# Kernel tuning notes

Measured on AMD Instinct MI355X. Metric: run time of the kernel, lower is better.

Reference implementation:

```python
import jax, jax.numpy as jnp
import numpy as np

N_EMBD = 1024
N_HEAD = 16
HEAD_DIM = N_EMBD // N_HEAD
B, T = 4, 2048


def setup_inputs() -> dict:
    key = jax.random.key(0)
    ks = jax.random.split(key, 5)
    s_in = 1.0 / np.sqrt(N_EMBD)
    return {
        "x": jax.random.normal(ks[0], (B, T, N_EMBD), dtype=jnp.float32),
        "w_attn": jax.random.normal(ks[1], (N_EMBD, 3 * N_EMBD), dtype=jnp.float32) * s_in,
        "b_attn": jnp.zeros((3 * N_EMBD,), dtype=jnp.float32),
        "w_proj": jax.random.normal(ks[2], (N_EMBD, N_EMBD), dtype=jnp.float32) * s_in,
        "b_proj": jnp.zeros((N_EMBD,), dtype=jnp.float32),
    }


def reference(x, w_attn, b_attn, w_proj, b_proj):
    b, t, c = x.shape
    qkv = x @ w_attn + b_attn                      # [B,T,3C]
    q, k, v = jnp.split(qkv, 3, axis=-1)
    # [B,T,C] -> [B,H,T,D]
    def heads(z):
        return z.reshape(b, t, N_HEAD, HEAD_DIM).transpose(0, 2, 1, 3)
    q, k, v = heads(q), heads(k), heads(v)
    scale = 1.0 / np.sqrt(HEAD_DIM)
    att = jnp.einsum("bhqd,bhkd->bhqk", q, k) * scale
    causal = jnp.tril(jnp.ones((t, t), dtype=bool))
    att = jnp.where(causal, att, -jnp.inf)
    att = jax.nn.softmax(att, axis=-1)
    y = jnp.einsum("bhqk,bhkd->bhqd", att, v)      # [B,H,T,D]
    y = y.transpose(0, 2, 1, 3).reshape(b, t, c)
    return y @ w_proj + b_proj
```

## Files before the change

### kernel.cpp

```cpp
#include <hip/hip_runtime.h>
#include <hip/hip_bf16.h>

#define B_  4
#define T_  2048
#define C_  1024
#define H_  16
#define D_  64
#define C3_ 3072

typedef __attribute__((ext_vector_type(8))) short bf16x8;
typedef __attribute__((ext_vector_type(4))) float f32x4;
typedef unsigned short u16;

#define CSCALE 0.1803368801111204f

__device__ __forceinline__ u16 f2bf(float f) {
  union { float f; unsigned int u; } v; v.f = f;
  unsigned int r = (v.u + 0x7FFFu + ((v.u >> 16) & 1u)) >> 16;
  return (u16)r;
}

__device__ __forceinline__ void gload16(void* l, const void* g) {
  __builtin_amdgcn_global_load_lds(
      (const __attribute__((address_space(1))) unsigned int*)g,
      (__attribute__((address_space(3))) unsigned int*)l, 16, 0, 0);
}

__global__ __launch_bounds__(256)
void cvt_bf16(const float* __restrict__ in, u16* __restrict__ out, int n8) {
  int i = blockIdx.x * 256 + threadIdx.x;
  if (i >= n8) return;
  float4 a = *(const float4*)(in + (size_t)i * 8);
  float4 b = *(const float4*)(in + (size_t)i * 8 + 4);
  ushort4 lo, hi;
  lo.x = f2bf(a.x); lo.y = f2bf(a.y); lo.z = f2bf(a.z); lo.w = f2bf(a.w);
  hi.x = f2bf(b.x); hi.y = f2bf(b.y); hi.z = f2bf(b.z); hi.w = f2bf(b.w);
  *(ushort4*)(out + (size_t)i * 8) = lo;
  *(ushort4*)(out + (size_t)i * 8 + 4) = hi;
}

__global__ __launch_bounds__(256)
void transcvt(const float* __restrict__ w, u16* __restrict__ wT, int K, int N) {
  int n  = blockIdx.x * 64 + (threadIdx.x & 63);
  int k0 = blockIdx.y * 16 + (threadIdx.x >> 6) * 4;
  float v0 = w[(size_t)(k0 + 0) * N + n];
  float v1 = w[(size_t)(k0 + 1) * N + n];
  float v2 = w[(size_t)(k0 + 2) * N + n];
  float v3 = w[(size_t)(k0 + 3) * N + n];
  ushort4 o; o.x = f2bf(v0); o.y = f2bf(v1); o.z = f2bf(v2); o.w = f2bf(v3);
  *(ushort4*)(wT + (size_t)n * K + k0) = o;
}

__global__ __launch_bounds__(256)
void vtrans(const u16* __restrict__ qkv, u16* __restrict__ vT) {
  const int bid = blockIdx.x;
  const int bh = bid >> 6, tc = bid & 63;
  const int d = threadIdx.x & 63, t4 = threadIdx.x >> 6;
  const int t8 = tc * 4 + t4;
  const int b = bh >> 4, h = bh & 15;
  const u16* src = qkv + (size_t)(b * T_ + t8 * 8) * C3_ + 2 * C_ + h * 64 + d;
  union { u16 a[8]; int4 v; } u;
#pragma unroll
  for (int e = 0; e < 8; ++e) u.a[e] = src[(size_t)e * C3_];
  *(int4*)(vT + ((size_t)bh * 64 + d) * T_ + t8 * 8) = u.v;
}

template <typename OutT, int BM>
__global__ __launch_bounds__(512, 2)
void gemm256(const u16* __restrict__ A, const u16* __restrict__ Bt,
             const float* __restrict__ bias, OutT* __restrict__ C,
             int M, int N, int K, int qscale_cols) {
  constexpr int AG = BM * 8;
  constexpr int S  = AG + 2048;
  constexpr int MF = BM / 64;
  constexpr int ALOADS = BM / 128;
  __shared__ int4 lds[2 * S];

  const int tid = threadIdx.x, lane = tid & 63, wid = tid >> 6;
  const int wr = wid >> 2, wc = wid & 3;
  const int row0 = blockIdx.y * BM, col0 = blockIdx.x * 256;

  f32x4 acc[2 * MF][4];
#pragma unroll
  for (int m = 0; m < 2 * MF; ++m)
#pragma unroll
    for (int nf = 0; nf < 4; ++nf) acc[m][nf] = (f32x4){0.f, 0.f, 0.f, 0.f};

  const u16* pA[2][ALOADS]; const u16* pB[2][2];
#pragma unroll
  for (int h = 0; h < 2; ++h) {
#pragma unroll
    for (int i = 0; i < ALOADS; ++i) {
      int g = h * (AG / 2) + i * 512 + tid;
      int rr = ((g >> 7) << 4) + (g & 15), ko = ((g >> 4) & 7) * 8;
      pA[h][i] = A + (size_t)(row0 + rr) * K + ko;
    }
#pragma unroll
    for (int i = 0; i < 2; ++i) {
      int g = h * 1024 + i * 512 + tid;
      int rr = ((g >> 7) << 4) + (g & 15), ko = ((g >> 4) & 7) * 8;
      pB[h][i] = Bt + (size_t)(col0 + rr) * K + ko;
    }
  }

  auto stage = [&](int t, int isA, int h, int buf) {
    if (isA) {
      int4* d = &lds[buf * S + h * (AG / 2) + wid * 64];
      gload16(d, pA[h][0] + t * 64);
      if constexpr (ALOADS == 2) gload16(d + 512, pA[h][1] + t * 64);
    } else {
      int4* d = &lds[buf * S + AG + h * 1024 + wid * 64];
      gload16(d, pB[h][0] + t * 64);
      gload16(d + 512, pB[h][1] + t * 64);
    }
  };
  auto rdA = [&](int f, int kk, int buf) {
    return *(const bf16x8*)&lds[buf * S + (wr * (2 * MF) + f) * 128 + kk * 64 + lane];
  };
  auto rdB = [&](int nf, int kk, int buf) {
    return *(const bf16x8*)&lds[buf * S + AG + (wc * 4 + nf) * 128 + kk * 64 + lane];
  };

#define WAIT_KEEP() do { if constexpr (BM == 256) \
    asm volatile("s_waitcnt vmcnt(6)" ::: "memory"); else \
    asm volatile("s_waitcnt vmcnt(5)" ::: "memory"); } while (0)

  const int nk = K >> 6, nit = nk >> 1;

  stage(0, 1, 0, 0); stage(0, 1, 1, 0); stage(0, 0, 0, 0); stage(0, 0, 1, 0);
  stage(1, 0, 0, 1); stage(1, 0, 1, 1); stage(1, 1, 0, 1);
  WAIT_KEEP();
  __builtin_amdgcn_s_barrier();

  for (int it = 0; it < nit; ++it) {
    const int t1g = 2 * it + 1, t2g = t1g + 1, t3g = t1g + 2;
    bf16x8 a0[MF][2], a1[MF][2], b0[2][2], b1[2][2];

#pragma unroll
    for (int m = 0; m < MF; ++m) { a0[m][0] = rdA(m, 0, 0); a0[m][1] = rdA(m, 1, 0); }
#pragma unroll
    for (int nf = 0; nf < 2; ++nf) { b0[nf][0] = rdB(nf, 0, 0); b0[nf][1] = rdB(nf, 1, 0); }
    stage(t1g, 1, 1, 1);
    __builtin_amdgcn_s_barrier();
    __builtin_amdgcn_s_setprio(1);
#pragma unroll
    for (int m = 0; m < MF; ++m)
#pragma unroll
      for (int nf = 0; nf < 2; ++nf) {
        acc[m][nf] = __builtin_amdgcn_mfma_f32_16x16x32_bf16(a0[m][0], b0[nf][0], acc[m][nf], 0, 0, 0);
        acc[m][nf] = __builtin_amdgcn_mfma_f32_16x16x32_bf16(a0[m][1], b0[nf][1], acc[m][nf], 0, 0, 0);
      }
    __builtin_amdgcn_s_setprio(0);
    __builtin_amdgcn_s_barrier();

#pragma unroll
    for (int nf = 0; nf < 2; ++nf) { b1[nf][0] = rdB(2 + nf, 0, 0); b1[nf][1] = rdB(2 + nf, 1, 0); }
    __builtin_amdgcn_s_barrier();
    __builtin_amdgcn_s_setprio(1);
#pragma unroll
    for (int m = 0; m < MF; ++m)
#pragma unroll
      for (int nf = 0; nf < 2; ++nf) {
        acc[m][2 + nf] = __builtin_amdgcn_mfma_f32_16x16x32_bf16(a0[m][0], b1[nf][0], acc[m][2 + nf], 0, 0, 0);
        acc[m][2 + nf] = __builtin_amdgcn_mfma_f32_16x16x32_bf16(a0[m][1], b1[nf][1], acc[m][2 + nf], 0, 0, 0);
      }
    __builtin_amdgcn_s_setprio(0);
    __builtin_amdgcn_s_barrier();

#pragma unroll
    for (int m = 0; m < MF; ++m) { a1[m][0] = rdA(MF + m, 0, 0); a1[m][1] = rdA(MF + m, 1, 0); }
    if (t2g < nk) stage(t2g, 0, 0, 0);
    __builtin_amdgcn_s_barrier();
    __builtin_amdgcn_s_setprio(1);
#pragma unroll
    for (int m = 0; m < MF; ++m)
#pragma unroll
      for (int nf = 0; nf < 2; ++nf) {
        acc[MF + m][2 + nf] = __builtin_amdgcn_mfma_f32_16x16x32_bf16(a1[m][0], b1[nf][0], acc[MF + m][2 + nf], 0, 0, 0);
        acc[MF + m][2 + nf] = __builtin_amdgcn_mfma_f32_16x16x32_bf16(a1[m][1], b1[nf][1], acc[MF + m][2 + nf], 0, 0, 0);
      }
    __builtin_amdgcn_s_setprio(0);
    __builtin_amdgcn_s_barrier();

    if (t2g < nk) {
      stage(t2g, 0, 1, 0);
      stage(t2g, 1, 0, 0);
      WAIT_KEEP();
    } else {
      asm volatile("s_waitcnt vmcnt(0)" ::: "memory");
    }
    __builtin_amdgcn_s_barrier();
    __builtin_amdgcn_s_setprio(1);
#pragma unroll
    for (int m = 0; m < MF; ++m)
#pragma unroll
      for (int nf = 0; nf < 2; ++nf) {
        acc[MF + m][nf] = __builtin_amdgcn_mfma_f32_16x16x32_bf16(a1[m][0], b0[nf][0], acc[MF + m][nf], 0, 0, 0);
        acc[MF + m][nf] = __builtin_amdgcn_mfma_f32_16x16x32_bf16(a1[m][1], b0[nf][1], acc[MF + m][nf], 0, 0, 0);
      }
    __builtin_amdgcn_s_setprio(0);
    __builtin_amdgcn_s_barrier();

#pragma unroll
    for (int m = 0; m < MF; ++m) { a0[m][0] = rdA(m, 0, 1); a0[m][1] = rdA(m, 1, 1); }
#pragma unroll
    for (int nf = 0; nf < 2; ++nf) { b0[nf][0] = rdB(nf, 0, 1); b0[nf][1] = rdB(nf, 1, 1); }
    if (t2g < nk) stage(t2g, 1, 1, 0);
    __builtin_amdgcn_s_barrier();
    __builtin_amdgcn_s_setprio(1);
#pragma unroll
    for (int m = 0; m < MF; ++m)
#pragma unroll
      for (int nf = 0; nf < 2; ++nf) {
        acc[m][nf] = __builtin_amdgcn_mfma_f32_16x16x32_bf16(a0[m][0], b0[nf][0], acc[m][nf], 0, 0, 0);
        acc[m][nf] = __builtin_amdgcn_mfma_f32_16x16x32_bf16(a0[m][1], b0[nf][1], acc[m][nf], 0, 0, 0);
      }
    __builtin_amdgcn_s_setprio(0);
    __builtin_amdgcn_s_barrier();

#pragma unroll
    for (int nf = 0; nf < 2; ++nf) { b1[nf][0] = rdB(2 + nf, 0, 1); b1[nf][1] = rdB(2 + nf, 1, 1); }
    __builtin_amdgcn_s_barrier();
    __builtin_amdgcn_s_setprio(1);
#pragma unroll
    for (int m = 0; m < MF; ++m)
#pragma unroll
      for (int nf = 0; nf < 2; ++nf) {
        acc[m][2 + nf] = __builtin_amdgcn_mfma_f32_16x16x32_bf16(a0[m][0], b1[nf][0], acc[m][2 + nf], 0, 0, 0);
        acc[m][2 + nf] = __builtin_amdgcn_mfma_f32_16x16x32_bf16(a0[m][1], b1[nf][1], acc[m][2 + nf], 0, 0, 0);
      }
    __builtin_amdgcn_s_setprio(0);
    __builtin_amdgcn_s_barrier();

#pragma unroll
    for (int m = 0; m < MF; ++m) { a1[m][0] = rdA(MF + m, 0, 1); a1[m][1] = rdA(MF + m, 1, 1); }
    if (t3g < nk) stage(t3g, 0, 0, 1);
    __builtin_amdgcn_s_barrier();
    __builtin_amdgcn_s_setprio(1);
#pragma unroll
    for (int m = 0; m < MF; ++m)
#pragma unroll
      for (int nf = 0; nf < 2; ++nf) {
        acc[MF + m][2 + nf] = __builtin_amdgcn_mfma_f32_16x16x32_bf16(a1[m][0], b1[nf][0], acc[MF + m][2 + nf], 0, 0, 0);
        acc[MF + m][2 + nf] = __builtin_amdgcn_mfma_f32_16x16x32_bf16(a1[m][1], b1[nf][1], acc[MF + m][2 + nf], 0, 0, 0);
      }
    __builtin_amdgcn_s_setprio(0);
    __builtin_amdgcn_s_barrier();

    if (t3g < nk) {
      stage(t3g, 0, 1, 1);
      stage(t3g, 1, 0, 1);
      WAIT_KEEP();
    } else {
      asm volatile("s_waitcnt vmcnt(0)" ::: "memory");
    }
    __builtin_amdgcn_s_barrier();
    __builtin_amdgcn_s_setprio(1);
#pragma unroll
    for (int m = 0; m < MF; ++m)
#pragma unroll
      for (int nf = 0; nf < 2; ++nf) {
        acc[MF + m][nf] = __builtin_amdgcn_mfma_f32_16x16x32_bf16(a1[m][0], b0[nf][0], acc[MF + m][nf], 0, 0, 0);
        acc[MF + m][nf] = __builtin_amdgcn_mfma_f32_16x16x32_bf16(a1[m][1], b0[nf][1], acc[MF + m][nf], 0, 0, 0);
      }
    __builtin_amdgcn_s_setprio(0);
    __builtin_amdgcn_s_barrier();
  }
#undef WAIT_KEEP

  const int cc = lane & 15, qg = lane >> 4;
#pragma unroll
  for (int m = 0; m < 2 * MF; ++m) {
#pragma unroll
    for (int nf = 0; nf < 4; ++nf) {
      const int gc = col0 + wc * 64 + nf * 16 + cc;
      const float bv = bias[gc];
      const float sc = (gc < qscale_cols) ? CSCALE : 1.0f;
#pragma unroll
      for (int r = 0; r < 4; ++r) {
        const int gr = row0 + wr * (BM / 2) + m * 16 + qg * 4 + r;
        float val = (acc[m][nf][r] + bv) * sc;
        if constexpr (sizeof(OutT) == 2)
          ((u16*)C)[(size_t)gr * N + gc] = f2bf(val);
        else
          ((float*)C)[(size_t)gr * N + gc] = val;
      }
    }
  }
}

__global__ __launch_bounds__(512, 4)
void attn_mfma(const u16* __restrict__ qkv, const u16* __restrict__ vT,
               u16* __restrict__ yout) {
  __shared__ int4 Ks4[512];
  __shared__ int4 Vs4[512];
  __shared__ int4 Ps4[2048];

  const int n   = blockIdx.x;
  const int xcd = n & 7, t = n >> 3;
  const int bh  = xcd * 8 + (t >> 3);
  const int ip  = t & 7;
  const int b   = bh >> 4, h = bh & 15;

  const int tid = threadIdx.x;
  const int lane = tid & 63, wq = tid >> 6;
  const int sub = wq & 3;
  const int cc = lane & 15, qg = lane >> 4;

  const int qt128 = (wq < 4) ? ip : (15 - ip);
  const int qrow0 = qt128 * 128 + sub * 32;
  const int diag  = qt128 * 2 + (sub >> 1);
  const int jn    = 32 - 2 * ip;

  const u16* kbase = qkv + (size_t)b * T_ * C3_ + C_ + h * D_;
  const u16* vtb   = vT + (size_t)bh * D_ * T_;

  bf16x8 qf[2][2];
#pragma unroll
  for (int hf = 0; hf < 2; ++hf) {
    const u16* qb = qkv + (size_t)(b * T_ + qrow0 + hf * 16 + cc) * C3_ + h * D_;
    qf[hf][0] = *(const bf16x8*)(qb + qg * 8);
    qf[hf][1] = *(const bf16x8*)(qb + 32 + qg * 8);
  }

  const u16* kg = kbase + (size_t)((tid >> 7) * 16 + (tid & 15)) * C3_ +
                  ((tid >> 6) & 1) * 32 + ((tid >> 4) & 3) * 8;
  const u16* vg = vtb + (size_t)((tid >> 7) * 16 + (tid & 15)) * T_ +
                  ((tid >> 6) & 1) * 32 + ((tid >> 4) & 3) * 8;

  int4 kpref = *(const int4*)kg;
  int4 vpref = *(const int4*)vg;

  float m_r[2] = {-1e30f, -1e30f}, l_r[2] = {0.f, 0.f};
  f32x4 o[2][4];
#pragma unroll
  for (int hf = 0; hf < 2; ++hf)
#pragma unroll
    for (int db = 0; db < 4; ++db) o[hf][db] = (f32x4){0.f, 0.f, 0.f, 0.f};

  for (int j = 0; j < jn; ++j) {
    __syncthreads();
    Ks4[tid] = kpref;
    Vs4[tid] = vpref;
    __syncthreads();
    if (j + 1 < jn) {
      kpref = *(const int4*)(kg + (size_t)(j + 1) * 64 * C3_);
      vpref = *(const int4*)(vg + (j + 1) * 64);
    }
    if (j > diag) continue;

    __builtin_amdgcn_s_setprio(1);
    f32x4 s[2][4];
#pragma unroll
    for (int kb = 0; kb < 4; ++kb) {
      bf16x8 kf0 = *(const bf16x8*)(Ks4 + kb * 128 + lane);
      bf16x8 kf1 = *(const bf16x8*)(Ks4 + kb * 128 + 64 + lane);
#pragma unroll
      for (int hf = 0; hf < 2; ++hf) {
        f32x4 z = (f32x4){0.f, 0.f, 0.f, 0.f};
        z = __builtin_amdgcn_mfma_f32_16x16x32_bf16(kf0, qf[hf][0], z, 0, 0, 0);
        z = __builtin_amdgcn_mfma_f32_16x16x32_bf16(kf1, qf[hf][1], z, 0, 0, 0);
        s[hf][kb] = z;
      }
    }
    __builtin_amdgcn_s_setprio(0);

    if (j == diag) {
#pragma unroll
      for (int hf = 0; hf < 2; ++hf) {
        const int qabs = qrow0 + hf * 16 + cc;
#pragma unroll
        for (int kb = 0; kb < 4; ++kb)
#pragma unroll
          for (int r = 0; r < 4; ++r)
            if ((j * 64 + kb * 16 + qg * 4 + r) > qabs) s[hf][kb][r] = -1e30f;
      }
    }

#pragma unroll
    for (int hf = 0; hf < 2; ++hf) {
      float mx = s[hf][0][0];
#pragma unroll
      for (int kb = 0; kb < 4; ++kb)
#pragma unroll
        for (int r = 0; r < 4; ++r) mx = fmaxf(mx, s[hf][kb][r]);
      mx = fmaxf(mx, __shfl_xor(mx, 16));
      mx = fmaxf(mx, __shfl_xor(mx, 32));

      if (!__all(mx <= m_r[hf])) {
        float mn = fmaxf(m_r[hf], mx);
        float al = exp2f(m_r[hf] - mn);
        m_r[hf] = mn;
        l_r[hf] *= al;
        float alq[4];
#pragma unroll
        for (int r = 0; r < 4; ++r)
          alq[r] = __shfl(al, (lane & 48) | (qg * 4 + r));
#pragma unroll
        for (int db = 0; db < 4; ++db)
#pragma unroll
          for (int r = 0; r < 4; ++r) o[hf][db][r] *= alq[r];
      }

      float lsum = 0.f;
#pragma unroll
      for (int kb = 0; kb < 4; ++kb)
#pragma unroll
        for (int r = 0; r < 4; ++r) {
          float p = exp2f(s[hf][kb][r] - m_r[hf]);
          s[hf][kb][r] = p;
          lsum += p;
        }
      l_r[hf] += lsum;

      char* myPb = (char*)(Ps4 + wq * 256 + hf * 128);
#pragma unroll
      for (int kb = 0; kb < 4; ++kb) {
        unsigned plo, phi;
        asm("v_cvt_pk_bf16_f32 %0, %1, %2" : "=v"(plo) : "v"(s[hf][kb][0]), "v"(s[hf][kb][1]));
        asm("v_cvt_pk_bf16_f32 %0, %1, %2" : "=v"(phi) : "v"(s[hf][kb][2]), "v"(s[hf][kb][3]));
        const int kv0 = kb * 16 + qg * 4;
        const int g = ((kv0 >> 5) << 6) + (((kv0 >> 3) & 3) << 4) + cc;
        uint2 pk; pk.x = plo; pk.y = phi;
        *(uint2*)(myPb + g * 16 + (kv0 & 7) * 2) = pk;
      }
    }

    bf16x8 pa[2][2];
#pragma unroll
    for (int hf = 0; hf < 2; ++hf)
#pragma unroll
      for (int ks = 0; ks < 2; ++ks)
        pa[hf][ks] = *(const bf16x8*)(Ps4 + wq * 256 + hf * 128 + ks * 64 + lane);
    __builtin_amdgcn_s_setprio(1);
#pragma unroll
    for (int db = 0; db < 4; ++db) {
#pragma unroll
      for (int ks = 0; ks < 2; ++ks) {
        bf16x8 vf = *(const bf16x8*)(Vs4 + db * 128 + ks * 64 + lane);
        o[0][db] = __builtin_amdgcn_mfma_f32_16x16x32_bf16(pa[0][ks], vf, o[0][db], 0, 0, 0);
        o[1][db] = __builtin_amdgcn_mfma_f32_16x16x32_bf16(pa[1][ks], vf, o[1][db], 0, 0, 0);
      }
    }
    __builtin_amdgcn_s_setprio(0);
  }

#pragma unroll
  for (int hf = 0; hf < 2; ++hf) {
    float ls = l_r[hf];
    ls += __shfl_xor(ls, 16);
    ls += __shfl_xor(ls, 32);
    float linv_l = 1.0f / ls;
    float linv[4];
#pragma unroll
    for (int r = 0; r < 4; ++r)
      linv[r] = __shfl(linv_l, (lane & 48) | (qg * 4 + r));

    u16* yb = yout + (size_t)(b * T_ + qrow0 + hf * 16 + qg * 4) * C_ + h * D_ + cc;
#pragma unroll
    for (int db = 0; db < 4; ++db)
#pragma unroll
      for (int r = 0; r < 4; ++r)
        yb[(size_t)r * C_ + db * 16] = f2bf(o[hf][db][r] * linv[r]);
  }
}

extern "C" void kernel_launch(void* const* d_in, const int* in_sizes, int n_in,
                              void* d_out, int out_size, void* d_ws, size_t ws_size,
                              hipStream_t stream) {
  const float* x      = (const float*)d_in[0];
  const float* w_attn = (const float*)d_in[1];
  const float* b_attn = (const float*)d_in[2];
  const float* w_proj = (const float*)d_in[3];
  const float* b_proj = (const float*)d_in[4];
  float* out = (float*)d_out;

  char* ws = (char*)d_ws;
  u16* xb  = (u16*)(ws);
  u16* waT = (u16*)(ws + 16777216);
  u16* wpT = (u16*)(ws + 23068672);
  u16* qkv = (u16*)(ws + 25165824);
  u16* yb  = (u16*)(ws + 75497472);
  u16* vT  = (u16*)(ws + 92274688);

  cvt_bf16<<<4096, 256, 0, stream>>>(x, xb, (B_ * T_ * C_) / 8);
  transcvt<<<dim3(C3_ / 64, C_ / 16), 256, 0, stream>>>(w_attn, waT, C_, C3_);
  transcvt<<<dim3(C_ / 64, C_ / 16), 256, 0, stream>>>(w_proj, wpT, C_, C_);

  gemm256<u16, 256><<<dim3(C3_ / 256, (B_ * T_) / 256), 512, 0, stream>>>(
      xb, waT, b_attn, qkv, B_ * T_, C3_, C_, C_);

  vtrans<<<4096, 256, 0, stream>>>(qkv, vT);

  attn_mfma<<<dim3(8 * H_ * B_), 512, 0, stream>>>(qkv, vT, yb);

  gemm256<float, 128><<<dim3(C_ / 256, (B_ * T_) / 128), 512, 0, stream>>>(
      yb, wpT, b_proj, out, B_ * T_, C_, C_, 0);
}
```

Before: 218.3 us.

## Double-buffer K/V tiles in LDS with direct global-to-LDS async loads

```diff
diff --git a/kernel.cpp b/kernel.cpp
--- a/kernel.cpp
+++ b/kernel.cpp
@@ -292,8 +292,8 @@
 __global__ __launch_bounds__(512, 4)
 void attn_mfma(const u16* __restrict__ qkv, const u16* __restrict__ vT,
                u16* __restrict__ yout) {
-  __shared__ int4 Ks4[512];
-  __shared__ int4 Vs4[512];
+  __shared__ int4 Ks4[2][512];
+  __shared__ int4 Vs4[2][512];
   __shared__ int4 Ps4[2048];
 
   const int n   = blockIdx.x;
@@ -328,9 +328,6 @@
   const u16* vg = vtb + (size_t)((tid >> 7) * 16 + (tid & 15)) * T_ +
                   ((tid >> 6) & 1) * 32 + ((tid >> 4) & 3) * 8;
 
-  int4 kpref = *(const int4*)kg;
-  int4 vpref = *(const int4*)vg;
-
   float m_r[2] = {-1e30f, -1e30f}, l_r[2] = {0.f, 0.f};
   f32x4 o[2][4];
 #pragma unroll
@@ -338,111 +335,116 @@
 #pragma unroll
     for (int db = 0; db < 4; ++db) o[hf][db] = (f32x4){0.f, 0.f, 0.f, 0.f};
 
+  gload16(&Ks4[0][wq * 64], kg);
+  gload16(&Vs4[0][wq * 64], vg);
+  __syncthreads();
+
   for (int j = 0; j < jn; ++j) {
+    const int p = j & 1;
+
+    if (j + 1 < jn) {
+      gload16(&Ks4[p ^ 1][wq * 64], kg + (size_t)(j + 1) * 64 * C3_);
+      gload16(&Vs4[p ^ 1][wq * 64], vg + (j + 1) * 64);
+    }
+
+    if (j <= diag) {
+      __builtin_amdgcn_s_setprio(1);
+      f32x4 s[2][4];
+#pragma unroll
+      for (int kb = 0; kb < 4; ++kb) {
+        bf16x8 kf0 = *(const bf16x8*)(&Ks4[p][0] + kb * 128 + lane);
+        bf16x8 kf1 = *(const bf16x8*)(&Ks4[p][0] + kb * 128 + 64 + lane);
+#pragma unroll
+        for (int hf = 0; hf < 2; ++hf) {
+          f32x4 z = (f32x4){0.f, 0.f, 0.f, 0.f};
+          z = __builtin_amdgcn_mfma_f32_16x16x32_bf16(kf0, qf[hf][0], z, 0, 0, 0);
+          z = __builtin_amdgcn_mfma_f32_16x16x32_bf16(kf1, qf[hf][1], z, 0, 0, 0);
+          s[hf][kb] = z;
+        }
+      }
+      __builtin_amdgcn_s_setprio(0);
+
+      if (j == diag) {
+#pragma unroll
+        for (int hf = 0; hf < 2; ++hf) {
+          const int qabs = qrow0 + hf * 16 + cc;
+#pragma unroll
+          for (int kb = 0; kb < 4; ++kb)
+#pragma unroll
+            for (int r = 0; r < 4; ++r)
+              if ((j * 64 + kb * 16 + qg * 4 + r) > qabs) s[hf][kb][r] = -1e30f;
+        }
+      }
+
+#pragma unroll
+      for (int hf = 0; hf < 2; ++hf) {
+        float m0 = fmaxf(fmaxf(s[hf][0][0], s[hf][0][1]), fmaxf(s[hf][0][2], s[hf][0][3]));
+        float m1 = fmaxf(fmaxf(s[hf][1][0], s[hf][1][1]), fmaxf(s[hf][1][2], s[hf][1][3]));
+        float m2 = fmaxf(fmaxf(s[hf][2][0], s[hf][2][1]), fmaxf(s[hf][2][2], s[hf][2][3]));
+        float m3 = fmaxf(fmaxf(s[hf][3][0], s[hf][3][1]), fmaxf(s[hf][3][2], s[hf][3][3]));
+        float mx = fmaxf(fmaxf(m0, m1), fmaxf(m2, m3));
+        mx = fmaxf(mx, __shfl_xor(mx, 16));
+        mx = fmaxf(mx, __shfl_xor(mx, 32));
+
+        if (!__all(mx <= m_r[hf])) {
+          float mn = fmaxf(m_r[hf], mx);
+          float al = exp2f(m_r[hf] - mn);
+          m_r[hf] = mn;
+          l_r[hf] *= al;
+          float alq[4];
+#pragma unroll
+          for (int r = 0; r < 4; ++r)
+            alq[r] = __shfl(al, (lane & 48) | (qg * 4 + r));
+#pragma unroll
+          for (int db = 0; db < 4; ++db)
+#pragma unroll
+            for (int r = 0; r < 4; ++r) o[hf][db][r] *= alq[r];
+        }
+
+#pragma unroll
+        for (int kb = 0; kb < 4; ++kb)
+#pragma unroll
+          for (int r = 0; r < 4; ++r)
+            s[hf][kb][r] = exp2f(s[hf][kb][r] - m_r[hf]);
+        float l0 = (s[hf][0][0] + s[hf][0][1]) + (s[hf][0][2] + s[hf][0][3]);
+        float l1 = (s[hf][1][0] + s[hf][1][1]) + (s[hf][1][2] + s[hf][1][3]);
+        float l2 = (s[hf][2][0] + s[hf][2][1]) + (s[hf][2][2] + s[hf][2][3]);
+        float l3 = (s[hf][3][0] + s[hf][3][1]) + (s[hf][3][2] + s[hf][3][3]);
+        l_r[hf] += (l0 + l1) + (l2 + l3);
+
+        char* myPb = (char*)(Ps4 + wq * 256 + hf * 128);
+#pragma unroll
+        for (int kb = 0; kb < 4; ++kb) {
+          unsigned plo, phi;
+          asm("v_cvt_pk_bf16_f32 %0, %1, %2" : "=v"(plo) : "v"(s[hf][kb][0]), "v"(s[hf][kb][1]));
+          asm("v_cvt_pk_bf16_f32 %0, %1, %2" : "=v"(phi) : "v"(s[hf][kb][2]), "v"(s[hf][kb][3]));
+          const int kv0 = kb * 16 + qg * 4;
+          const int g = ((kv0 >> 5) << 6) + (((kv0 >> 3) & 3) << 4) + cc;
+          uint2 pk; pk.x = plo; pk.y = phi;
+          *(uint2*)(myPb + g * 16 + (kv0 & 7) * 2) = pk;
+        }
+      }
+
+      bf16x8 pa[2][2];
+#pragma unroll
+      for (int hf = 0; hf < 2; ++hf)
+#pragma unroll
+        for (int ks = 0; ks < 2; ++ks)
+          pa[hf][ks] = *(const bf16x8*)(Ps4 + wq * 256 + hf * 128 + ks * 64 + lane);
+      __builtin_amdgcn_s_setprio(1);
+#pragma unroll
+      for (int db = 0; db < 4; ++db) {
+#pragma unroll
+        for (int ks = 0; ks < 2; ++ks) {
+          bf16x8 vf = *(const bf16x8*)(&Vs4[p][0] + db * 128 + ks * 64 + lane);
+          o[0][db] = __builtin_amdgcn_mfma_f32_16x16x32_bf16(pa[0][ks], vf, o[0][db], 0, 0, 0);
+          o[1][db] = __builtin_amdgcn_mfma_f32_16x16x32_bf16(pa[1][ks], vf, o[1][db], 0, 0, 0);
+        }
+      }
+      __builtin_amdgcn_s_setprio(0);
+    }
+
     __syncthreads();
-    Ks4[tid] = kpref;
-    Vs4[tid] = vpref;
-    __syncthreads();
-    if (j + 1 < jn) {
-      kpref = *(const int4*)(kg + (size_t)(j + 1) * 64 * C3_);
-      vpref = *(const int4*)(vg + (j + 1) * 64);
-    }
-    if (j > diag) continue;
-
-    __builtin_amdgcn_s_setprio(1);
-    f32x4 s[2][4];
-#pragma unroll
-    for (int kb = 0; kb < 4; ++kb) {
-      bf16x8 kf0 = *(const bf16x8*)(Ks4 + kb * 128 + lane);
-      bf16x8 kf1 = *(const bf16x8*)(Ks4 + kb * 128 + 64 + lane);
-#pragma unroll
-      for (int hf = 0; hf < 2; ++hf) {
-        f32x4 z = (f32x4){0.f, 0.f, 0.f, 0.f};
-        z = __builtin_amdgcn_mfma_f32_16x16x32_bf16(kf0, qf[hf][0], z, 0, 0, 0);
-        z = __builtin_amdgcn_mfma_f32_16x16x32_bf16(kf1, qf[hf][1], z, 0, 0, 0);
-        s[hf][kb] = z;
-      }
-    }
-    __builtin_amdgcn_s_setprio(0);
-
-    if (j == diag) {
-#pragma unroll
-      for (int hf = 0; hf < 2; ++hf) {
-        const int qabs = qrow0 + hf * 16 + cc;
-#pragma unroll
-        for (int kb = 0; kb < 4; ++kb)
-#pragma unroll
-          for (int r = 0; r < 4; ++r)
-            if ((j * 64 + kb * 16 + qg * 4 + r) > qabs) s[hf][kb][r] = -1e30f;
-      }
-    }
-
-#pragma unroll
-    for (int hf = 0; hf < 2; ++hf) {
-      float mx = s[hf][0][0];
-#pragma unroll
-      for (int kb = 0; kb < 4; ++kb)
-#pragma unroll
-        for (int r = 0; r < 4; ++r) mx = fmaxf(mx, s[hf][kb][r]);
-      mx = fmaxf(mx, __shfl_xor(mx, 16));
-      mx = fmaxf(mx, __shfl_xor(mx, 32));
-
-      if (!__all(mx <= m_r[hf])) {
-        float mn = fmaxf(m_r[hf], mx);
-        float al = exp2f(m_r[hf] - mn);
-        m_r[hf] = mn;
-        l_r[hf] *= al;
-        float alq[4];
-#pragma unroll
-        for (int r = 0; r < 4; ++r)
-          alq[r] = __shfl(al, (lane & 48) | (qg * 4 + r));
-#pragma unroll
-        for (int db = 0; db < 4; ++db)
-#pragma unroll
-          for (int r = 0; r < 4; ++r) o[hf][db][r] *= alq[r];
-      }
-
-      float lsum = 0.f;
-#pragma unroll
-      for (int kb = 0; kb < 4; ++kb)
-#pragma unroll
-        for (int r = 0; r < 4; ++r) {
-          float p = exp2f(s[hf][kb][r] - m_r[hf]);
-          s[hf][kb][r] = p;
-          lsum += p;
-        }
-      l_r[hf] += lsum;
-
-      char* myPb = (char*)(Ps4 + wq * 256 + hf * 128);
-#pragma unroll
-      for (int kb = 0; kb < 4; ++kb) {
-        unsigned plo, phi;
-        asm("v_cvt_pk_bf16_f32 %0, %1, %2" : "=v"(plo) : "v"(s[hf][kb][0]), "v"(s[hf][kb][1]));
-        asm("v_cvt_pk_bf16_f32 %0, %1, %2" : "=v"(phi) : "v"(s[hf][kb][2]), "v"(s[hf][kb][3]));
-        const int kv0 = kb * 16 + qg * 4;
-        const int g = ((kv0 >> 5) << 6) + (((kv0 >> 3) & 3) << 4) + cc;
-        uint2 pk; pk.x = plo; pk.y = phi;
-        *(uint2*)(myPb + g * 16 + (kv0 & 7) * 2) = pk;
-      }
-    }
-
-    bf16x8 pa[2][2];
-#pragma unroll
-    for (int hf = 0; hf < 2; ++hf)
-#pragma unroll
-      for (int ks = 0; ks < 2; ++ks)
-        pa[hf][ks] = *(const bf16x8*)(Ps4 + wq * 256 + hf * 128 + ks * 64 + lane);
-    __builtin_amdgcn_s_setprio(1);
-#pragma unroll
-    for (int db = 0; db < 4; ++db) {
-#pragma unroll
-      for (int ks = 0; ks < 2; ++ks) {
-        bf16x8 vf = *(const bf16x8*)(Vs4 + db * 128 + ks * 64 + lane);
-        o[0][db] = __builtin_amdgcn_mfma_f32_16x16x32_bf16(pa[0][ks], vf, o[0][db], 0, 0, 0);
-        o[1][db] = __builtin_amdgcn_mfma_f32_16x16x32_bf16(pa[1][ks], vf, o[1][db], 0, 0, 0);
-      }
-    }
-    __builtin_amdgcn_s_setprio(0);
   }
 
 #pragma unroll
```

Result: slower. 227.8 us (+4.4%).

## Fuse V transpose into QKV GEMM epilogue and merge weight transpose kernels

Applied to the files above, without the earlier changes.

```diff
diff --git a/kernel.cpp b/kernel.cpp
--- a/kernel.cpp
+++ b/kernel.cpp
@@ -40,36 +40,26 @@
 }
 
 __global__ __launch_bounds__(256)
-void transcvt(const float* __restrict__ w, u16* __restrict__ wT, int K, int N) {
-  int n  = blockIdx.x * 64 + (threadIdx.x & 63);
-  int k0 = blockIdx.y * 16 + (threadIdx.x >> 6) * 4;
+void transcvt2(const float* __restrict__ wa, u16* __restrict__ waT,
+               const float* __restrict__ wp, u16* __restrict__ wpT) {
+  const int bx = blockIdx.x;
+  const float* w; u16* wT; int N, n;
+  if (bx < 48) { w = wa; wT = waT; N = C3_; n = bx * 64 + (threadIdx.x & 63); }
+  else         { w = wp; wT = wpT; N = C_;  n = (bx - 48) * 64 + (threadIdx.x & 63); }
+  const int k0 = blockIdx.y * 16 + (threadIdx.x >> 6) * 4;
   float v0 = w[(size_t)(k0 + 0) * N + n];
   float v1 = w[(size_t)(k0 + 1) * N + n];
   float v2 = w[(size_t)(k0 + 2) * N + n];
   float v3 = w[(size_t)(k0 + 3) * N + n];
   ushort4 o; o.x = f2bf(v0); o.y = f2bf(v1); o.z = f2bf(v2); o.w = f2bf(v3);
-  *(ushort4*)(wT + (size_t)n * K + k0) = o;
-}
-
-__global__ __launch_bounds__(256)
-void vtrans(const u16* __restrict__ qkv, u16* __restrict__ vT) {
-  const int bid = blockIdx.x;
-  const int bh = bid >> 6, tc = bid & 63;
-  const int d = threadIdx.x & 63, t4 = threadIdx.x >> 6;
-  const int t8 = tc * 4 + t4;
-  const int b = bh >> 4, h = bh & 15;
-  const u16* src = qkv + (size_t)(b * T_ + t8 * 8) * C3_ + 2 * C_ + h * 64 + d;
-  union { u16 a[8]; int4 v; } u;
-#pragma unroll
-  for (int e = 0; e < 8; ++e) u.a[e] = src[(size_t)e * C3_];
-  *(int4*)(vT + ((size_t)bh * 64 + d) * T_ + t8 * 8) = u.v;
-}
-
-template <typename OutT, int BM>
+  *(ushort4*)(wT + (size_t)n * 1024 + k0) = o;
+}
+
+template <typename OutT, int BM, bool VSPLIT>
 __global__ __launch_bounds__(512, 2)
 void gemm256(const u16* __restrict__ A, const u16* __restrict__ Bt,
              const float* __restrict__ bias, OutT* __restrict__ C,
-             int M, int N, int K, int qscale_cols) {
+             u16* __restrict__ vTout, int M, int N, int K, int qscale_cols) {
   constexpr int AG = BM * 8;
   constexpr int S  = AG + 2048;
   constexpr int MF = BM / 64;
@@ -275,15 +265,26 @@
     for (int nf = 0; nf < 4; ++nf) {
       const int gc = col0 + wc * 64 + nf * 16 + cc;
       const float bv = bias[gc];
-      const float sc = (gc < qscale_cols) ? CSCALE : 1.0f;
-#pragma unroll
-      for (int r = 0; r < 4; ++r) {
-        const int gr = row0 + wr * (BM / 2) + m * 16 + qg * 4 + r;
-        float val = (acc[m][nf][r] + bv) * sc;
-        if constexpr (sizeof(OutT) == 2)
-          ((u16*)C)[(size_t)gr * N + gc] = f2bf(val);
-        else
-          ((float*)C)[(size_t)gr * N + gc] = val;
+      const int gr0 = row0 + wr * (BM / 2) + m * 16 + qg * 4;
+      if (VSPLIT && gc >= 2 * C_) {
+        const int hh = (gc - 2 * C_) >> 6, d = (gc - 2 * C_) & 63;
+        const int bb = gr0 >> 11, tloc = gr0 & 2047;
+        ushort4 pk;
+        pk.x = f2bf(acc[m][nf][0] + bv);
+        pk.y = f2bf(acc[m][nf][1] + bv);
+        pk.z = f2bf(acc[m][nf][2] + bv);
+        pk.w = f2bf(acc[m][nf][3] + bv);
+        *(ushort4*)(vTout + ((size_t)(bb * 16 + hh) * 64 + d) * T_ + tloc) = pk;
+      } else {
+        const float sc = (gc < qscale_cols) ? CSCALE : 1.0f;
+#pragma unroll
+        for (int r = 0; r < 4; ++r) {
+          float val = (acc[m][nf][r] + bv) * sc;
+          if constexpr (sizeof(OutT) == 2)
+            ((u16*)C)[(size_t)(gr0 + r) * N + gc] = f2bf(val);
+          else
+            ((float*)C)[(size_t)(gr0 + r) * N + gc] = val;
+        }
       }
     }
   }
@@ -484,16 +485,13 @@
   u16* vT  = (u16*)(ws + 92274688);
 
   cvt_bf16<<<4096, 256, 0, stream>>>(x, xb, (B_ * T_ * C_) / 8);
-  transcvt<<<dim3(C3_ / 64, C_ / 16), 256, 0, stream>>>(w_attn, waT, C_, C3_);
-  transcvt<<<dim3(C_ / 64, C_ / 16), 256, 0, stream>>>(w_proj, wpT, C_, C_);
-
-  gemm256<u16, 256><<<dim3(C3_ / 256, (B_ * T_) / 256), 512, 0, stream>>>(
-      xb, waT, b_attn, qkv, B_ * T_, C3_, C_, C_);
-
-  vtrans<<<4096, 256, 0, stream>>>(qkv, vT);
+  transcvt2<<<dim3(64, 64), 256, 0, stream>>>(w_attn, waT, w_proj, wpT);
+
+  gemm256<u16, 256, true><<<dim3(C3_ / 256, (B_ * T_) / 256), 512, 0, stream>>>(
+      xb, waT, b_attn, qkv, vT, B_ * T_, C3_, C_, C_);
 
   attn_mfma<<<dim3(8 * H_ * B_), 512, 0, stream>>>(qkv, vT, yb);
 
-  gemm256<float, 128><<<dim3(C_ / 256, (B_ * T_) / 128), 512, 0, stream>>>(
-      yb, wpT, b_proj, out, B_ * T_, C_, C_, 0);
-}
+  gemm256<float, 128, false><<<dim3(C_ / 256, (B_ * T_) / 128), 512, 0, stream>>>(
+      yb, wpT, b_proj, out, nullptr, B_ * T_, C_, C_, 0);
+}
```

New measurement: 211.8 us. 1.03x faster.
